# Optimization experiments

Hardware: AMD Instinct MI355X
Metric: run time of the kernel (lower is better)

The kernel has to match this reference:

```python
import jax, jax.numpy as jnp
import numpy as np

B, L, DIM, H = 2, 2048, 1024, 16
HD = DIM // H  # 64
EPS = 1e-6
ROPE_THETA = 10000.0


def _rmsnorm(x, scale):
    # mean of squares in float32 as in torch (dtype=torch.float32)
    ms = jnp.mean(jnp.square(x.astype(jnp.float32)), axis=-1, keepdims=True)
    inv = jax.lax.rsqrt(ms + EPS).astype(x.dtype)
    return x * inv * scale.astype(x.dtype)


def _rope_cos_sin(seq_len, head_dim, dtype):
    inv_freq = 1.0 / (ROPE_THETA ** (jnp.arange(0, head_dim, 2, dtype=jnp.float32) / head_dim))
    ang = jnp.arange(seq_len, dtype=jnp.float32)[:, None] * inv_freq[None, :]  # [L, HD/2]
    cos = jnp.cos(ang)[:, None, :].astype(dtype)  # [L,1,HD/2] broadcast over heads
    sin = jnp.sin(ang)[:, None, :].astype(dtype)
    return cos, sin


def _rope_apply(x, cos, sin):
    # x: [B,L,H,HD]; rotate-half formulation
    x1, x2 = jnp.split(x, 2, axis=-1)
    return jnp.concatenate([x1 * cos - x2 * sin, x2 * cos + x1 * sin], axis=-1)


def setup_inputs() -> dict:
    key = jax.random.key(0)
    k1, k2, k3 = jax.random.split(key, 3)
    x = jax.random.normal(k1, (B, L, DIM), dtype=jnp.float32)
    Wqkv = jax.random.normal(k2, (DIM, 3 * DIM), dtype=jnp.float32) * (DIM ** -0.5)
    Wproj = jax.random.normal(k3, (DIM, DIM), dtype=jnp.float32) * (DIM ** -0.5)
    q_scale = jnp.ones((HD,), dtype=jnp.float32)
    k_scale = jnp.ones((HD,), dtype=jnp.float32)
    bproj = jnp.zeros((DIM,), dtype=jnp.float32)
    return {"x": x, "Wqkv": Wqkv, "q_scale": q_scale, "k_scale": k_scale,
            "Wproj": Wproj, "bproj": bproj}


def reference(x, Wqkv, q_scale, k_scale, Wproj, bproj):
    b, l, c = x.shape
    qkv = x @ Wqkv  # [B,L,3*DIM]
    qkv = qkv.reshape(b, l, 3, H, HD)
    q, k, v = qkv[:, :, 0], qkv[:, :, 1], qkv[:, :, 2]  # each [B,L,H,HD]
    q = _rmsnorm(q, q_scale)
    k = _rmsnorm(k, k_scale)
    cos, sin = _rope_cos_sin(l, HD, x.dtype)
    q = _rope_apply(q, cos, sin)
    k = _rope_apply(k, cos, sin)
    scale = HD ** -0.5
    scores = jnp.einsum('blhd,bmhd->bhlm', q, k) * scale  # [B,H,L,L]
    p = jax.nn.softmax(scores, axis=-1)
    o = jnp.einsum('bhlm,bmhd->blhd', p, v).reshape(b, l, c)
    return o @ Wproj + bproj
```

## Files before the change

### kernel.cpp

```cpp
#include <hip/hip_runtime.h>
#include <hip/hip_bf16.h>
#include <cstdint>

#define B_   2
#define L_   2048
#define DIM_ 1024
#define H_   16
#define HD_  64
#define M_   (B_ * L_)
#define N3_  (3 * DIM_)

typedef unsigned short ushort_t;
typedef __bf16 bf16x8 __attribute__((ext_vector_type(8)));
typedef float  f32x4  __attribute__((ext_vector_type(4)));

__device__ __forceinline__ unsigned short f2b(float f) {
  return __builtin_bit_cast(unsigned short, (__bf16)f);
}
__device__ __forceinline__ float b2f(unsigned short s) {
  unsigned u = ((unsigned)s) << 16;
  return __builtin_bit_cast(float, u);
}
__device__ __forceinline__ float fmax3(float a, float b, float c) {
  return fmaxf(fmaxf(a, b), c);
}

typedef const __attribute__((address_space(1))) void* as1cp;
typedef __attribute__((address_space(3))) void* as3p;
__device__ __forceinline__ void gload_lds16(const void* g, void* l) {
  __builtin_amdgcn_global_load_lds((as1cp)g, (as3p)l, 16, 0, 0);
}

__global__ __launch_bounds__(256)
void conv_bf16(const float* __restrict__ in, ushort_t* __restrict__ out, int n4) {
  int i = blockIdx.x * 256 + threadIdx.x;
  if (i >= n4) return;
  float4 v = *(const float4*)&in[(size_t)i * 4];
  ushort4 o;
  o.x = f2b(v.x); o.y = f2b(v.y); o.z = f2b(v.z); o.w = f2b(v.w);
  *(ushort4*)&out[(size_t)i * 4] = o;
}

__global__ __launch_bounds__(256)
void transpose_conv(const float* __restrict__ in, ushort_t* __restrict__ out,
                    int R, int C) {
  __shared__ float tile[64][65];
  const int t = threadIdx.x;
  const int r0 = blockIdx.y * 64, c0 = blockIdx.x * 64;
#pragma unroll
  for (int p = 0; p < 4; ++p) {
    int r = (t >> 4) + p * 16;
    int c = (t & 15) * 4;
    float4 v = *(const float4*)&in[(size_t)(r0 + r) * C + (c0 + c)];
    tile[r][c + 0] = v.x; tile[r][c + 1] = v.y;
    tile[r][c + 2] = v.z; tile[r][c + 3] = v.w;
  }
  __syncthreads();
#pragma unroll
  for (int p = 0; p < 4; ++p) {
    int cc = (t >> 4) + p * 16;
    int r  = (t & 15) * 4;
    ushort4 o;
    o.x = f2b(tile[r + 0][cc]); o.y = f2b(tile[r + 1][cc]);
    o.z = f2b(tile[r + 2][cc]); o.w = f2b(tile[r + 3][cc]);
    *(ushort4*)&out[(size_t)(c0 + cc) * R + (r0 + r)] = o;
  }
}

__global__ __launch_bounds__(256)
void rope_tab(float* __restrict__ cosT, float* __restrict__ sinT) {
  int idx = blockIdx.x * 256 + threadIdx.x;
  int l = idx >> 5, d = idx & 31;
  float inv_freq = expf(-((float)(2 * d) / 64.f) * logf(10000.f));
  float ang = (float)l * inv_freq;
  cosT[idx] = cosf(ang);
  sinT[idx] = sinf(ang);
}

template <int MODE>
__global__ __launch_bounds__(256)
void gemm_bt(const ushort_t* __restrict__ A, const ushort_t* __restrict__ BT,
             void* __restrict__ Cout, ushort_t* __restrict__ vtout,
             const float* __restrict__ bias, int M, int N, int K, int ldc) {
  __shared__ ushort_t As[128 * 32];
  __shared__ ushort_t Bs[128 * 32];
  const int lane = threadIdx.x & 63;
  const int wid  = threadIdx.x >> 6;
  const int wm = wid >> 1, wn = wid & 1;
  const int m0 = blockIdx.y * 128, n0 = blockIdx.x * 128;
  const int ro = lane & 15, kg = lane >> 4;

  f32x4 acc[4][4] = {};

  for (int k0 = 0; k0 < K; k0 += 32) {
    const int cb = wid * 128;
#pragma unroll
    for (int j = 0; j < 2; ++j) {
      int c = cb + j * 64 + lane;
      gload_lds16(A + (size_t)(m0 + (c >> 2)) * K + k0 + (c & 3) * 8,
                  &As[(cb + j * 64) * 8]);
    }
#pragma unroll
    for (int j = 0; j < 2; ++j) {
      int c = cb + j * 64 + lane;
      gload_lds16(BT + (size_t)(n0 + (c >> 2)) * K + k0 + (c & 3) * 8,
                  &Bs[(cb + j * 64) * 8]);
    }
    __syncthreads();
    bf16x8 af[4], bfr[4];
#pragma unroll
    for (int i = 0; i < 4; ++i)
      af[i] = *(const bf16x8*)&As[(wm * 64 + i * 16 + ro) * 32 + kg * 8];
#pragma unroll
    for (int i = 0; i < 4; ++i)
      bfr[i] = *(const bf16x8*)&Bs[(wn * 64 + i * 16 + ro) * 32 + kg * 8];
#pragma unroll
    for (int i = 0; i < 4; ++i)
#pragma unroll
      for (int j = 0; j < 4; ++j)
        acc[i][j] = __builtin_amdgcn_mfma_f32_16x16x32_bf16(af[i], bfr[j],
                                                            acc[i][j], 0, 0, 0);
    __syncthreads();
  }

  if (MODE == 0) {
    if (n0 < 2048) {
#pragma unroll
      for (int i = 0; i < 4; ++i)
#pragma unroll
        for (int r = 0; r < 4; ++r) {
          int row = m0 + wm * 64 + i * 16 + kg * 4 + r;
#pragma unroll
          for (int j = 0; j < 4; ++j) {
            int col = n0 + wn * 64 + j * 16 + ro;
            ((ushort_t*)Cout)[(size_t)row * ldc + col] = f2b(acc[i][j][r]);
          }
        }
    } else {
#pragma unroll
      for (int i = 0; i < 4; ++i) {
        int rowb = m0 + wm * 64 + i * 16 + kg * 4;
        int bb = rowb >> 11, l = rowb & (L_ - 1);
#pragma unroll
        for (int j = 0; j < 4; ++j) {
          int dg = (n0 - 2048) + wn * 64 + j * 16 + ro;
          ushort4 o;
          o.x = f2b(acc[i][j][0]); o.y = f2b(acc[i][j][1]);
          o.z = f2b(acc[i][j][2]); o.w = f2b(acc[i][j][3]);
          *(ushort4*)&vtout[((size_t)bb * DIM_ + dg) * L_ + l] = o;
        }
      }
    }
  } else {
#pragma unroll
    for (int i = 0; i < 4; ++i)
#pragma unroll
      for (int r = 0; r < 4; ++r) {
        int row = m0 + wm * 64 + i * 16 + kg * 4 + r;
#pragma unroll
        for (int j = 0; j < 4; ++j) {
          int col = n0 + wn * 64 + j * 16 + ro;
          ((float*)Cout)[(size_t)row * ldc + col] = acc[i][j][r] + bias[col];
        }
      }
  }
}

__global__ __launch_bounds__(256)
void rmsrope(ushort_t* __restrict__ qk, const float* __restrict__ qs,
             const float* __restrict__ ks, const float* __restrict__ cosT,
             const float* __restrict__ sinT) {
  const int t = blockIdx.x;
  const int l = t & (L_ - 1);
  const int j = threadIdx.x & 15;
  const int h = threadIdx.x >> 4;
  const int dd = (j & 7) * 4;
  float4 cv = *(const float4*)&cosT[l * 32 + dd];
  float4 sv = *(const float4*)&sinT[l * 32 + dd];
  const float sgn = (j < 8) ? -1.f : 1.f;
#pragma unroll
  for (int ic = 0; ic < 2; ++ic) {
    const float qsc = (ic == 0) ? 0.125f * 1.44269504088896341f : 1.f;
    ushort_t* base = qk + (size_t)t * 2048 + ic * DIM_ + h * HD_ + j * 4;
    ushort4 raw = *(const ushort4*)base;
    float x0 = b2f(raw.x), x1 = b2f(raw.y), x2 = b2f(raw.z), x3 = b2f(raw.w);
    float ss = x0 * x0 + x1 * x1 + x2 * x2 + x3 * x3;
    ss += __shfl_xor(ss, 1); ss += __shfl_xor(ss, 2);
    ss += __shfl_xor(ss, 4); ss += __shfl_xor(ss, 8);
    float inv = rsqrtf(ss * (1.f / 64.f) + 1e-6f);
    const float* scp = (ic == 0 ? qs : ks) + j * 4;
    float4 sc = *(const float4*)scp;
    x0 *= inv * sc.x; x1 *= inv * sc.y; x2 *= inv * sc.z; x3 *= inv * sc.w;
    float y0 = __shfl_xor(x0, 8), y1 = __shfl_xor(x1, 8);
    float y2 = __shfl_xor(x2, 8), y3 = __shfl_xor(x3, 8);
    ushort4 o;
    o.x = f2b((x0 * cv.x + sgn * y0 * sv.x) * qsc);
    o.y = f2b((x1 * cv.y + sgn * y1 * sv.y) * qsc);
    o.z = f2b((x2 * cv.z + sgn * y2 * sv.z) * qsc);
    o.w = f2b((x3 * cv.w + sgn * y3 * sv.w) * qsc);
    *(ushort4*)base = o;
  }
}

__global__ __launch_bounds__(256)
void flash_attn(const ushort_t* __restrict__ qk, const ushort_t* __restrict__ vt,
                ushort_t* __restrict__ O) {
  const int qt = blockIdx.x, h = blockIdx.y, b = blockIdx.z;
  const int lane = threadIdx.x & 63, wid = threadIdx.x >> 6;
  const int ro = lane & 15, kg = lane >> 4;
  const int q0 = qt * 64;
  const size_t tok0 = (size_t)b * L_;
  const ushort_t* qb = qk + tok0 * 2048 + h * HD_;
  const ushort_t* kb = qb + DIM_;
  const ushort_t* vb = vt + ((size_t)b * DIM_ + h * HD_) * L_;

  __shared__ ushort_t Ks[2][4096];
  __shared__ ushort_t Vs[2][4096];
  __shared__ ushort_t Ps[4096];

  const int srow0 = wid * 16 + (lane >> 3);
  const int sch   = lane & 7;
  auto STAGE = [&](int bufi, int kt) {
#pragma unroll
    for (int j = 0; j < 2; ++j) {
      int row = srow0 + j * 8;
      int sc  = sch ^ (row & 7);
      gload_lds16(kb + (size_t)(kt * 64 + row) * 2048 + sc * 8,
                  &Ks[bufi][wid * 1024 + j * 512]);
      gload_lds16(vb + (size_t)row * L_ + kt * 64 + sc * 8,
                  &Vs[bufi][wid * 1024 + j * 512]);
    }
  };

  bf16x8 qf[2];
  {
    const ushort_t* g = qb + (size_t)(q0 + wid * 16 + ro) * 2048 + kg * 8;
    qf[0] = *(const bf16x8*)g;
    qf[1] = *(const bf16x8*)(g + 32);
  }

  bf16x8 onesv;
#pragma unroll
  for (int i = 0; i < 8; ++i) onesv[i] = (__bf16)1.0f;

  f32x4 oacc[4] = {};
  f32x4 lacc = {0.f, 0.f, 0.f, 0.f};
  float mrow = -1e30f;

  const int rowq = wid * 16 + ro;
  const int rx = ro & 7;

  const ushort_t* kbase[2][2];
  const ushort_t* vbase[2][2];
#pragma unroll
  for (int bi = 0; bi < 2; ++bi)
#pragma unroll
    for (int kk = 0; kk < 2; ++kk) {
      int ch = (kk * 4 + kg) ^ rx;
      kbase[bi][kk] = &Ks[bi][ro * 64 + ch * 8];
      vbase[bi][kk] = &Vs[bi][ro * 64 + ch * 8];
    }
  const ushort_t* pbase[2];
#pragma unroll
  for (int kk = 0; kk < 2; ++kk)
    pbase[kk] = &Ps[rowq * 64 + (((kk * 4 + kg) ^ rx) * 8)];
  ushort_t* pwaddr[4];
#pragma unroll
  for (int n = 0; n < 4; ++n)
    pwaddr[n] = &Ps[rowq * 64 + (((n * 2 + (kg >> 1)) ^ rx) * 8) + (kg & 1) * 4];

  STAGE(0, 0);
  __syncthreads();

  auto TILE = [&](int bi, int kt) {
    if (kt + 1 < L_ / 64) STAGE(bi ^ 1, kt + 1);

    f32x4 s[4];
#pragma unroll
    for (int n = 0; n < 4; ++n) {
      f32x4 z = {0.f, 0.f, 0.f, 0.f};
#pragma unroll
      for (int kk = 0; kk < 2; ++kk) {
        bf16x8 kf = *(const bf16x8*)(kbase[bi][kk] + n * 1024);
        z = __builtin_amdgcn_mfma_f32_16x16x32_bf16(kf, qf[kk], z, 0, 0, 0);
      }
      s[n] = z;
    }

    float t0 = fmax3(s[0][0], s[0][1], s[0][2]);
    float t1 = fmax3(s[0][3], s[1][0], s[1][1]);
    float t2 = fmax3(s[1][2], s[1][3], s[2][0]);
    float t3 = fmax3(s[2][1], s[2][2], s[2][3]);
    float t4 = fmax3(s[3][0], s[3][1], s[3][2]);
    float pm  = fmax3(t0, t1, t2);
    float pm2 = fmax3(t3, t4, s[3][3]);
    pm = fmaxf(pm, pm2);
    pm = fmaxf(pm, __shfl_xor(pm, 16));
    pm = fmaxf(pm, __shfl_xor(pm, 32));

    if (__any(pm > mrow + 8.f)) {
      float mn = fmaxf(mrow, pm);
      float alpha = __builtin_amdgcn_exp2f(mrow - mn);
      mrow = mn;
      float aro[4];
#pragma unroll
      for (int r = 0; r < 4; ++r) aro[r] = __shfl(alpha, kg * 20 + r);
#pragma unroll
      for (int n = 0; n < 4; ++n)
#pragma unroll
        for (int r = 0; r < 4; ++r) oacc[n][r] *= aro[r];
#pragma unroll
      for (int r = 0; r < 4; ++r) lacc[r] *= aro[r];
    }

#pragma unroll
    for (int n = 0; n < 4; ++n) {
      ushort4 pw;
      pw.x = f2b(__builtin_amdgcn_exp2f(s[n][0] - mrow));
      pw.y = f2b(__builtin_amdgcn_exp2f(s[n][1] - mrow));
      pw.z = f2b(__builtin_amdgcn_exp2f(s[n][2] - mrow));
      pw.w = f2b(__builtin_amdgcn_exp2f(s[n][3] - mrow));
      *(ushort4*)pwaddr[n] = pw;
    }

#pragma unroll
    for (int kk = 0; kk < 2; ++kk) {
      bf16x8 pf = *(const bf16x8*)pbase[kk];
      lacc = __builtin_amdgcn_mfma_f32_16x16x32_bf16(pf, onesv, lacc, 0, 0, 0);
#pragma unroll
      for (int n = 0; n < 4; ++n) {
        bf16x8 vf = *(const bf16x8*)(vbase[bi][kk] + n * 1024);
        oacc[n] = __builtin_amdgcn_mfma_f32_16x16x32_bf16(pf, vf, oacc[n], 0, 0, 0);
      }
    }

    __syncthreads();
  };

  for (int kt = 0; kt < L_ / 64; kt += 2) {
    TILE(0, kt);
    TILE(1, kt + 1);
  }

  float linv[4];
#pragma unroll
  for (int r = 0; r < 4; ++r) linv[r] = 1.f / lacc[r];
#pragma unroll
  for (int r = 0; r < 4; ++r) {
    int tok = (int)tok0 + q0 + wid * 16 + kg * 4 + r;
#pragma unroll
    for (int n = 0; n < 4; ++n)
      O[(size_t)tok * DIM_ + h * HD_ + n * 16 + ro] = f2b(oacc[n][r] * linv[r]);
  }
}

extern "C" void kernel_launch(void* const* d_in, const int* in_sizes, int n_in,
                              void* d_out, int out_size, void* d_ws, size_t ws_size,
                              hipStream_t stream) {
  const float* x     = (const float*)d_in[0];
  const float* Wqkv  = (const float*)d_in[1];
  const float* qs    = (const float*)d_in[2];
  const float* ks    = (const float*)d_in[3];
  const float* Wproj = (const float*)d_in[4];
  const float* bproj = (const float*)d_in[5];
  float* out = (float*)d_out;

  char* ws = (char*)d_ws;
  ushort_t* xb     = (ushort_t*)(ws);
  ushort_t* WqkvT  = (ushort_t*)(ws + (size_t)(8u << 20));
  ushort_t* WprojT = (ushort_t*)(ws + (size_t)(14u << 20));
  ushort_t* qkb    = (ushort_t*)(ws + (size_t)(16u << 20));
  ushort_t* vtb    = (ushort_t*)(ws + (size_t)(32u << 20));
  float*    cosT   = (float*)(ws + (size_t)(40u << 20));
  float*    sinT   = (float*)(ws + (size_t)(40u << 20) + (256u << 10));
  ushort_t* ob     = (ushort_t*)(ws + (size_t)(41u << 20));

  conv_bf16<<<4096, 256, 0, stream>>>(x, xb, M_ * DIM_ / 4);
  transpose_conv<<<dim3(48, 16), 256, 0, stream>>>(Wqkv, WqkvT, DIM_, N3_);
  transpose_conv<<<dim3(16, 16), 256, 0, stream>>>(Wproj, WprojT, DIM_, DIM_);
  rope_tab<<<256, 256, 0, stream>>>(cosT, sinT);
  gemm_bt<0><<<dim3(24, 32), 256, 0, stream>>>(xb, WqkvT, qkb, vtb, nullptr,
                                               M_, N3_, DIM_, 2048);
  rmsrope<<<4096, 256, 0, stream>>>(qkb, qs, ks, cosT, sinT);
  flash_attn<<<dim3(32, 16, 2), 256, 0, stream>>>(qkb, vtb, ob);
  gemm_bt<1><<<dim3(8, 32), 256, 0, stream>>>(ob, WprojT, out, nullptr, bproj,
                                              M_, DIM_, DIM_, DIM_);
}
```

Before: 159.7 us.

## Process two query row groups per wave in flash attention for K/V reuse

```diff
diff --git a/kernel.cpp b/kernel.cpp
--- a/kernel.cpp
+++ b/kernel.cpp
@@ -208,7 +208,7 @@
   const int qt = blockIdx.x, h = blockIdx.y, b = blockIdx.z;
   const int lane = threadIdx.x & 63, wid = threadIdx.x >> 6;
   const int ro = lane & 15, kg = lane >> 4;
-  const int q0 = qt * 64;
+  const int q0 = qt * 128;
   const size_t tok0 = (size_t)b * L_;
   const ushort_t* qb = qk + tok0 * 2048 + h * HD_;
   const ushort_t* kb = qb + DIM_;
@@ -216,7 +216,7 @@
 
   __shared__ ushort_t Ks[2][4096];
   __shared__ ushort_t Vs[2][4096];
-  __shared__ ushort_t Ps[4096];
+  __shared__ ushort_t Ps[8192];
 
   const int srow0 = wid * 16 + (lane >> 3);
   const int sch   = lane & 7;
@@ -232,22 +232,22 @@
     }
   };
 
-  bf16x8 qf[2];
-  {
-    const ushort_t* g = qb + (size_t)(q0 + wid * 16 + ro) * 2048 + kg * 8;
-    qf[0] = *(const bf16x8*)g;
-    qf[1] = *(const bf16x8*)(g + 32);
+  bf16x8 qf[2][2];
+#pragma unroll
+  for (int g = 0; g < 2; ++g) {
+    const ushort_t* gp = qb + (size_t)(q0 + wid * 32 + g * 16 + ro) * 2048 + kg * 8;
+    qf[g][0] = *(const bf16x8*)gp;
+    qf[g][1] = *(const bf16x8*)(gp + 32);
   }
 
   bf16x8 onesv;
 #pragma unroll
   for (int i = 0; i < 8; ++i) onesv[i] = (__bf16)1.0f;
 
-  f32x4 oacc[4] = {};
-  f32x4 lacc = {0.f, 0.f, 0.f, 0.f};
-  float mrow = -1e30f;
-
-  const int rowq = wid * 16 + ro;
+  f32x4 oacc[2][4] = {};
+  f32x4 lacc[2] = {};
+  float mrow[2] = {-1e30f, -1e30f};
+
   const int rx = ro & 7;
 
   const ushort_t* kbase[2][2];
@@ -260,14 +260,18 @@
       kbase[bi][kk] = &Ks[bi][ro * 64 + ch * 8];
       vbase[bi][kk] = &Vs[bi][ro * 64 + ch * 8];
     }
-  const ushort_t* pbase[2];
-#pragma unroll
-  for (int kk = 0; kk < 2; ++kk)
-    pbase[kk] = &Ps[rowq * 64 + (((kk * 4 + kg) ^ rx) * 8)];
-  ushort_t* pwaddr[4];
-#pragma unroll
-  for (int n = 0; n < 4; ++n)
-    pwaddr[n] = &Ps[rowq * 64 + (((n * 2 + (kg >> 1)) ^ rx) * 8) + (kg & 1) * 4];
+  const ushort_t* pbase[2][2];
+  ushort_t* pwaddr[2][4];
+#pragma unroll
+  for (int g = 0; g < 2; ++g) {
+    const int rowq = wid * 32 + g * 16 + ro;
+#pragma unroll
+    for (int kk = 0; kk < 2; ++kk)
+      pbase[g][kk] = &Ps[rowq * 64 + (((kk * 4 + kg) ^ rx) * 8)];
+#pragma unroll
+    for (int n = 0; n < 4; ++n)
+      pwaddr[g][n] = &Ps[rowq * 64 + (((n * 2 + (kg >> 1)) ^ rx) * 8) + (kg & 1) * 4];
+  }
 
   STAGE(0, 0);
   __syncthreads();
@@ -275,64 +279,76 @@
   auto TILE = [&](int bi, int kt) {
     if (kt + 1 < L_ / 64) STAGE(bi ^ 1, kt + 1);
 
-    f32x4 s[4];
+    f32x4 s[2][4];
+    __builtin_amdgcn_s_setprio(1);
 #pragma unroll
     for (int n = 0; n < 4; ++n) {
-      f32x4 z = {0.f, 0.f, 0.f, 0.f};
+      f32x4 z0 = {0.f, 0.f, 0.f, 0.f};
+      f32x4 z1 = {0.f, 0.f, 0.f, 0.f};
 #pragma unroll
       for (int kk = 0; kk < 2; ++kk) {
         bf16x8 kf = *(const bf16x8*)(kbase[bi][kk] + n * 1024);
-        z = __builtin_amdgcn_mfma_f32_16x16x32_bf16(kf, qf[kk], z, 0, 0, 0);
-      }
-      s[n] = z;
-    }
-
-    float t0 = fmax3(s[0][0], s[0][1], s[0][2]);
-    float t1 = fmax3(s[0][3], s[1][0], s[1][1]);
-    float t2 = fmax3(s[1][2], s[1][3], s[2][0]);
-    float t3 = fmax3(s[2][1], s[2][2], s[2][3]);
-    float t4 = fmax3(s[3][0], s[3][1], s[3][2]);
-    float pm  = fmax3(t0, t1, t2);
-    float pm2 = fmax3(t3, t4, s[3][3]);
-    pm = fmaxf(pm, pm2);
-    pm = fmaxf(pm, __shfl_xor(pm, 16));
-    pm = fmaxf(pm, __shfl_xor(pm, 32));
-
-    if (__any(pm > mrow + 8.f)) {
-      float mn = fmaxf(mrow, pm);
-      float alpha = __builtin_amdgcn_exp2f(mrow - mn);
-      mrow = mn;
-      float aro[4];
-#pragma unroll
-      for (int r = 0; r < 4; ++r) aro[r] = __shfl(alpha, kg * 20 + r);
-#pragma unroll
-      for (int n = 0; n < 4; ++n)
-#pragma unroll
-        for (int r = 0; r < 4; ++r) oacc[n][r] *= aro[r];
-#pragma unroll
-      for (int r = 0; r < 4; ++r) lacc[r] *= aro[r];
-    }
-
-#pragma unroll
-    for (int n = 0; n < 4; ++n) {
-      ushort4 pw;
-      pw.x = f2b(__builtin_amdgcn_exp2f(s[n][0] - mrow));
-      pw.y = f2b(__builtin_amdgcn_exp2f(s[n][1] - mrow));
-      pw.z = f2b(__builtin_amdgcn_exp2f(s[n][2] - mrow));
-      pw.w = f2b(__builtin_amdgcn_exp2f(s[n][3] - mrow));
-      *(ushort4*)pwaddr[n] = pw;
-    }
-
+        z0 = __builtin_amdgcn_mfma_f32_16x16x32_bf16(kf, qf[0][kk], z0, 0, 0, 0);
+        z1 = __builtin_amdgcn_mfma_f32_16x16x32_bf16(kf, qf[1][kk], z1, 0, 0, 0);
+      }
+      s[0][n] = z0; s[1][n] = z1;
+    }
+    __builtin_amdgcn_s_setprio(0);
+
+#pragma unroll
+    for (int g = 0; g < 2; ++g) {
+      float t0 = fmax3(s[g][0][0], s[g][0][1], s[g][0][2]);
+      float t1 = fmax3(s[g][0][3], s[g][1][0], s[g][1][1]);
+      float t2 = fmax3(s[g][1][2], s[g][1][3], s[g][2][0]);
+      float t3 = fmax3(s[g][2][1], s[g][2][2], s[g][2][3]);
+      float t4 = fmax3(s[g][3][0], s[g][3][1], s[g][3][2]);
+      float pm  = fmax3(t0, t1, t2);
+      float pm2 = fmax3(t3, t4, s[g][3][3]);
+      pm = fmaxf(pm, pm2);
+      pm = fmaxf(pm, __shfl_xor(pm, 16));
+      pm = fmaxf(pm, __shfl_xor(pm, 32));
+
+      if (__any(pm > mrow[g] + 8.f)) {
+        float mn = fmaxf(mrow[g], pm);
+        float alpha = __builtin_amdgcn_exp2f(mrow[g] - mn);
+        mrow[g] = mn;
+        float aro[4];
+#pragma unroll
+        for (int r = 0; r < 4; ++r) aro[r] = __shfl(alpha, kg * 20 + r);
+#pragma unroll
+        for (int n = 0; n < 4; ++n)
+#pragma unroll
+          for (int r = 0; r < 4; ++r) oacc[g][n][r] *= aro[r];
+#pragma unroll
+        for (int r = 0; r < 4; ++r) lacc[g][r] *= aro[r];
+      }
+
+#pragma unroll
+      for (int n = 0; n < 4; ++n) {
+        ushort4 pw;
+        pw.x = f2b(__builtin_amdgcn_exp2f(s[g][n][0] - mrow[g]));
+        pw.y = f2b(__builtin_amdgcn_exp2f(s[g][n][1] - mrow[g]));
+        pw.z = f2b(__builtin_amdgcn_exp2f(s[g][n][2] - mrow[g]));
+        pw.w = f2b(__builtin_amdgcn_exp2f(s[g][n][3] - mrow[g]));
+        *(ushort4*)pwaddr[g][n] = pw;
+      }
+    }
+
+    __builtin_amdgcn_s_setprio(1);
 #pragma unroll
     for (int kk = 0; kk < 2; ++kk) {
-      bf16x8 pf = *(const bf16x8*)pbase[kk];
-      lacc = __builtin_amdgcn_mfma_f32_16x16x32_bf16(pf, onesv, lacc, 0, 0, 0);
+      bf16x8 pf0 = *(const bf16x8*)pbase[0][kk];
+      bf16x8 pf1 = *(const bf16x8*)pbase[1][kk];
+      lacc[0] = __builtin_amdgcn_mfma_f32_16x16x32_bf16(pf0, onesv, lacc[0], 0, 0, 0);
+      lacc[1] = __builtin_amdgcn_mfma_f32_16x16x32_bf16(pf1, onesv, lacc[1], 0, 0, 0);
 #pragma unroll
       for (int n = 0; n < 4; ++n) {
         bf16x8 vf = *(const bf16x8*)(vbase[bi][kk] + n * 1024);
-        oacc[n] = __builtin_amdgcn_mfma_f32_16x16x32_bf16(pf, vf, oacc[n], 0, 0, 0);
-      }
-    }
+        oacc[0][n] = __builtin_amdgcn_mfma_f32_16x16x32_bf16(pf0, vf, oacc[0][n], 0, 0, 0);
+        oacc[1][n] = __builtin_amdgcn_mfma_f32_16x16x32_bf16(pf1, vf, oacc[1][n], 0, 0, 0);
+      }
+    }
+    __builtin_amdgcn_s_setprio(0);
 
     __syncthreads();
   };
@@ -342,15 +358,18 @@
     TILE(1, kt + 1);
   }
 
-  float linv[4];
-#pragma unroll
-  for (int r = 0; r < 4; ++r) linv[r] = 1.f / lacc[r];
-#pragma unroll
-  for (int r = 0; r < 4; ++r) {
-    int tok = (int)tok0 + q0 + wid * 16 + kg * 4 + r;
-#pragma unroll
-    for (int n = 0; n < 4; ++n)
-      O[(size_t)tok * DIM_ + h * HD_ + n * 16 + ro] = f2b(oacc[n][r] * linv[r]);
+#pragma unroll
+  for (int g = 0; g < 2; ++g) {
+    float linv[4];
+#pragma unroll
+    for (int r = 0; r < 4; ++r) linv[r] = 1.f / lacc[g][r];
+#pragma unroll
+    for (int r = 0; r < 4; ++r) {
+      int tok = (int)tok0 + q0 + wid * 32 + g * 16 + kg * 4 + r;
+#pragma unroll
+      for (int n = 0; n < 4; ++n)
+        O[(size_t)tok * DIM_ + h * HD_ + n * 16 + ro] = f2b(oacc[g][n][r] * linv[r]);
+    }
   }
 }
 
@@ -382,7 +401,7 @@
   gemm_bt<0><<<dim3(24, 32), 256, 0, stream>>>(xb, WqkvT, qkb, vtb, nullptr,
                                                M_, N3_, DIM_, 2048);
   rmsrope<<<4096, 256, 0, stream>>>(qkb, qs, ks, cosT, sinT);
-  flash_attn<<<dim3(32, 16, 2), 256, 0, stream>>>(qkb, vtb, ob);
+  flash_attn<<<dim3(16, 16, 2), 256, 0, stream>>>(qkb, vtb, ob);
   gemm_bt<1><<<dim3(8, 32), 256, 0, stream>>>(ob, WprojT, out, nullptr, bproj,
                                               M_, DIM_, DIM_, DIM_);
 }
```

Result: faster. 150.9 us (-5.5%).

## Rewrite flash attention with 32x32 MFMA, register-resident P via permlane swap

Applied to the files above, without the earlier changes.

```diff
diff --git a/kernel.cpp b/kernel.cpp
--- a/kernel.cpp
+++ b/kernel.cpp
@@ -13,6 +13,8 @@
 typedef unsigned short ushort_t;
 typedef __bf16 bf16x8 __attribute__((ext_vector_type(8)));
 typedef float  f32x4  __attribute__((ext_vector_type(4)));
+typedef float  f32x16 __attribute__((ext_vector_type(16)));
+typedef unsigned u32x2_t __attribute__((ext_vector_type(2)));
 
 __device__ __forceinline__ unsigned short f2b(float f) {
   return __builtin_bit_cast(unsigned short, (__bf16)f);
@@ -23,6 +25,20 @@
 }
 __device__ __forceinline__ float fmax3(float a, float b, float c) {
   return fmaxf(fmaxf(a, b), c);
+}
+
+__device__ __forceinline__ void plswap(unsigned &a, unsigned &b) {
+#if defined(__has_builtin) && __has_builtin(__builtin_amdgcn_permlane32_swap)
+  u32x2_t r = __builtin_amdgcn_permlane32_swap(a, b, false, false);
+  a = r[0]; b = r[1];
+#else
+  unsigned sa = (unsigned)__shfl_xor((int)a, 32);
+  unsigned sb = (unsigned)__shfl_xor((int)b, 32);
+  bool hi = (threadIdx.x & 32) != 0;
+  unsigned na = hi ? sb : a;
+  unsigned nb = hi ? b : sa;
+  a = na; b = nb;
+#endif
 }
 
 typedef const __attribute__((address_space(1))) void* as1cp;
@@ -207,8 +223,9 @@
                 ushort_t* __restrict__ O) {
   const int qt = blockIdx.x, h = blockIdx.y, b = blockIdx.z;
   const int lane = threadIdx.x & 63, wid = threadIdx.x >> 6;
-  const int ro = lane & 15, kg = lane >> 4;
-  const int q0 = qt * 64;
+  const int lq = lane & 31;
+  const int hi = lane >> 5;
+  const int q0 = qt * 128;
   const size_t tok0 = (size_t)b * L_;
   const ushort_t* qb = qk + tok0 * 2048 + h * HD_;
   const ushort_t* kb = qb + DIM_;
@@ -216,7 +233,6 @@
 
   __shared__ ushort_t Ks[2][4096];
   __shared__ ushort_t Vs[2][4096];
-  __shared__ ushort_t Ps[4096];
 
   const int srow0 = wid * 16 + (lane >> 3);
   const int sch   = lane & 7;
@@ -232,107 +248,106 @@
     }
   };
 
-  bf16x8 qf[2];
+  bf16x8 qf[4];
   {
-    const ushort_t* g = qb + (size_t)(q0 + wid * 16 + ro) * 2048 + kg * 8;
-    qf[0] = *(const bf16x8*)g;
-    qf[1] = *(const bf16x8*)(g + 32);
-  }
-
-  bf16x8 onesv;
-#pragma unroll
-  for (int i = 0; i < 8; ++i) onesv[i] = (__bf16)1.0f;
-
-  f32x4 oacc[4] = {};
-  f32x4 lacc = {0.f, 0.f, 0.f, 0.f};
-  float mrow = -1e30f;
-
-  const int rowq = wid * 16 + ro;
-  const int rx = ro & 7;
-
-  const ushort_t* kbase[2][2];
-  const ushort_t* vbase[2][2];
-#pragma unroll
-  for (int bi = 0; bi < 2; ++bi)
-#pragma unroll
-    for (int kk = 0; kk < 2; ++kk) {
-      int ch = (kk * 4 + kg) ^ rx;
-      kbase[bi][kk] = &Ks[bi][ro * 64 + ch * 8];
-      vbase[bi][kk] = &Vs[bi][ro * 64 + ch * 8];
-    }
-  const ushort_t* pbase[2];
-#pragma unroll
-  for (int kk = 0; kk < 2; ++kk)
-    pbase[kk] = &Ps[rowq * 64 + (((kk * 4 + kg) ^ rx) * 8)];
-  ushort_t* pwaddr[4];
-#pragma unroll
-  for (int n = 0; n < 4; ++n)
-    pwaddr[n] = &Ps[rowq * 64 + (((n * 2 + (kg >> 1)) ^ rx) * 8) + (kg & 1) * 4];
+    const ushort_t* gp = qb + (size_t)(q0 + wid * 32 + lq) * 2048;
+#pragma unroll
+    for (int s = 0; s < 4; ++s)
+      qf[s] = *(const bf16x8*)(gp + s * 16 + hi * 8);
+  }
+
+  int chs[4];
+#pragma unroll
+  for (int s = 0; s < 4; ++s) chs[s] = ((2 * s + hi) ^ (lq & 7)) * 8;
+
+  f32x16 oaccT[2] = {};
+  float mrow = -1e30f, lrow = 0.f;
 
   STAGE(0, 0);
   __syncthreads();
 
   auto TILE = [&](int bi, int kt) {
     if (kt + 1 < L_ / 64) STAGE(bi ^ 1, kt + 1);
-
-    f32x4 s[4];
-#pragma unroll
-    for (int n = 0; n < 4; ++n) {
-      f32x4 z = {0.f, 0.f, 0.f, 0.f};
-#pragma unroll
-      for (int kk = 0; kk < 2; ++kk) {
-        bf16x8 kf = *(const bf16x8*)(kbase[bi][kk] + n * 1024);
-        z = __builtin_amdgcn_mfma_f32_16x16x32_bf16(kf, qf[kk], z, 0, 0, 0);
+    const ushort_t* kb0 = &Ks[bi][lq * 64];
+    const ushort_t* vb0 = &Vs[bi][lq * 64];
+
+    f32x16 st[2];
+    __builtin_amdgcn_s_setprio(1);
+#pragma unroll
+    for (int t = 0; t < 2; ++t) {
+      f32x16 z = {};
+#pragma unroll
+      for (int s = 0; s < 4; ++s) {
+        bf16x8 kf = *(const bf16x8*)(kb0 + t * 2048 + chs[s]);
+        z = __builtin_amdgcn_mfma_f32_32x32x16_bf16(kf, qf[s], z, 0, 0, 0);
       }
-      s[n] = z;
-    }
-
-    float t0 = fmax3(s[0][0], s[0][1], s[0][2]);
-    float t1 = fmax3(s[0][3], s[1][0], s[1][1]);
-    float t2 = fmax3(s[1][2], s[1][3], s[2][0]);
-    float t3 = fmax3(s[2][1], s[2][2], s[2][3]);
-    float t4 = fmax3(s[3][0], s[3][1], s[3][2]);
-    float pm  = fmax3(t0, t1, t2);
-    float pm2 = fmax3(t3, t4, s[3][3]);
-    pm = fmaxf(pm, pm2);
-    pm = fmaxf(pm, __shfl_xor(pm, 16));
-    pm = fmaxf(pm, __shfl_xor(pm, 32));
+      st[t] = z;
+    }
+    __builtin_amdgcn_s_setprio(0);
+
+    float mx0, mx1, mx2, mx3;
+    {
+      float a0 = fmaxf(fmaxf(st[0][0], st[0][1]),  fmaxf(st[0][2], st[0][3]));
+      float a1 = fmaxf(fmaxf(st[0][4], st[0][5]),  fmaxf(st[0][6], st[0][7]));
+      float a2 = fmaxf(fmaxf(st[0][8], st[0][9]),  fmaxf(st[0][10], st[0][11]));
+      float a3 = fmaxf(fmaxf(st[0][12], st[0][13]), fmaxf(st[0][14], st[0][15]));
+      float b0 = fmaxf(fmaxf(st[1][0], st[1][1]),  fmaxf(st[1][2], st[1][3]));
+      float b1 = fmaxf(fmaxf(st[1][4], st[1][5]),  fmaxf(st[1][6], st[1][7]));
+      float b2 = fmaxf(fmaxf(st[1][8], st[1][9]),  fmaxf(st[1][10], st[1][11]));
+      float b3 = fmaxf(fmaxf(st[1][12], st[1][13]), fmaxf(st[1][14], st[1][15]));
+      mx0 = fmaxf(a0, b0); mx1 = fmaxf(a1, b1);
+      mx2 = fmaxf(a2, b2); mx3 = fmaxf(a3, b3);
+    }
+    float pmw = fmaxf(fmax3(mx0, mx1, mx2), mx3);
+    float pm  = fmaxf(pmw, __shfl_xor(pmw, 32));
 
     if (__any(pm > mrow + 8.f)) {
       float mn = fmaxf(mrow, pm);
       float alpha = __builtin_amdgcn_exp2f(mrow - mn);
       mrow = mn;
-      float aro[4];
-#pragma unroll
-      for (int r = 0; r < 4; ++r) aro[r] = __shfl(alpha, kg * 20 + r);
-#pragma unroll
-      for (int n = 0; n < 4; ++n)
-#pragma unroll
-        for (int r = 0; r < 4; ++r) oacc[n][r] *= aro[r];
-#pragma unroll
-      for (int r = 0; r < 4; ++r) lacc[r] *= aro[r];
-    }
-
-#pragma unroll
-    for (int n = 0; n < 4; ++n) {
-      ushort4 pw;
-      pw.x = f2b(__builtin_amdgcn_exp2f(s[n][0] - mrow));
-      pw.y = f2b(__builtin_amdgcn_exp2f(s[n][1] - mrow));
-      pw.z = f2b(__builtin_amdgcn_exp2f(s[n][2] - mrow));
-      pw.w = f2b(__builtin_amdgcn_exp2f(s[n][3] - mrow));
-      *(ushort4*)pwaddr[n] = pw;
-    }
-
-#pragma unroll
-    for (int kk = 0; kk < 2; ++kk) {
-      bf16x8 pf = *(const bf16x8*)pbase[kk];
-      lacc = __builtin_amdgcn_mfma_f32_16x16x32_bf16(pf, onesv, lacc, 0, 0, 0);
-#pragma unroll
-      for (int n = 0; n < 4; ++n) {
-        bf16x8 vf = *(const bf16x8*)(vbase[bi][kk] + n * 1024);
-        oacc[n] = __builtin_amdgcn_mfma_f32_16x16x32_bf16(pf, vf, oacc[n], 0, 0, 0);
+      lrow *= alpha;
+#pragma unroll
+      for (int dt = 0; dt < 2; ++dt)
+#pragma unroll
+        for (int r = 0; r < 16; ++r) oaccT[dt][r] *= alpha;
+    }
+
+    unsigned pk[2][8];
+    float rs0 = 0.f, rs1 = 0.f, rs2 = 0.f, rs3 = 0.f;
+#pragma unroll
+    for (int t = 0; t < 2; ++t)
+#pragma unroll
+      for (int p = 0; p < 8; ++p) {
+        float e0 = __builtin_amdgcn_exp2f(st[t][2 * p]     - mrow);
+        float e1 = __builtin_amdgcn_exp2f(st[t][2 * p + 1] - mrow);
+        if ((p & 3) == 0) { rs0 += e0; rs1 += e1; }
+        else if ((p & 3) == 1) { rs2 += e0; rs3 += e1; }
+        else if ((p & 3) == 2) { rs0 += e0; rs1 += e1; }
+        else { rs2 += e0; rs3 += e1; }
+        pk[t][p] = (unsigned)f2b(e0) | ((unsigned)f2b(e1) << 16);
       }
-    }
+    lrow += (rs0 + rs1) + (rs2 + rs3);
+
+    __builtin_amdgcn_s_setprio(1);
+#pragma unroll
+    for (int t = 0; t < 2; ++t)
+#pragma unroll
+      for (int blk = 0; blk < 2; ++blk) {
+        unsigned w0 = pk[t][4 * blk + 0], w1 = pk[t][4 * blk + 1];
+        unsigned w2 = pk[t][4 * blk + 2], w3 = pk[t][4 * blk + 3];
+        plswap(w0, w2);
+        plswap(w1, w3);
+        uint4 bw; bw.x = w0; bw.y = w1; bw.z = w2; bw.w = w3;
+        bf16x8 pf = __builtin_bit_cast(bf16x8, bw);
+        const int sg = 2 * t + blk;
+#pragma unroll
+        for (int dt = 0; dt < 2; ++dt) {
+          bf16x8 vf = *(const bf16x8*)(vb0 + dt * 2048 + chs[sg]);
+          oaccT[dt] = __builtin_amdgcn_mfma_f32_32x32x16_bf16(vf, pf,
+                                                              oaccT[dt], 0, 0, 0);
+        }
+      }
+    __builtin_amdgcn_s_setprio(0);
 
     __syncthreads();
   };
@@ -342,16 +357,21 @@
     TILE(1, kt + 1);
   }
 
-  float linv[4];
-#pragma unroll
-  for (int r = 0; r < 4; ++r) linv[r] = 1.f / lacc[r];
-#pragma unroll
-  for (int r = 0; r < 4; ++r) {
-    int tok = (int)tok0 + q0 + wid * 16 + kg * 4 + r;
-#pragma unroll
-    for (int n = 0; n < 4; ++n)
-      O[(size_t)tok * DIM_ + h * HD_ + n * 16 + ro] = f2b(oacc[n][r] * linv[r]);
-  }
+  lrow += __shfl_xor(lrow, 32);
+  float linv = 1.f / lrow;
+  ushort_t* obp = O + (size_t)(tok0 + q0 + wid * 32 + lq) * DIM_ + h * HD_;
+#pragma unroll
+  for (int dt = 0; dt < 2; ++dt)
+#pragma unroll
+    for (int g4 = 0; g4 < 4; ++g4) {
+      int d0 = dt * 32 + g4 * 8 + hi * 4;
+      ushort4 o4;
+      o4.x = f2b(oaccT[dt][4 * g4 + 0] * linv);
+      o4.y = f2b(oaccT[dt][4 * g4 + 1] * linv);
+      o4.z = f2b(oaccT[dt][4 * g4 + 2] * linv);
+      o4.w = f2b(oaccT[dt][4 * g4 + 3] * linv);
+      *(ushort4*)(obp + d0) = o4;
+    }
 }
 
 extern "C" void kernel_launch(void* const* d_in, const int* in_sizes, int n_in,
@@ -382,7 +402,7 @@
   gemm_bt<0><<<dim3(24, 32), 256, 0, stream>>>(xb, WqkvT, qkb, vtb, nullptr,
                                                M_, N3_, DIM_, 2048);
   rmsrope<<<4096, 256, 0, stream>>>(qkb, qs, ks, cosT, sinT);
-  flash_attn<<<dim3(32, 16, 2), 256, 0, stream>>>(qkb, vtb, ob);
+  flash_attn<<<dim3(16, 16, 2), 256, 0, stream>>>(qkb, vtb, ob);
   gemm_bt<1><<<dim3(8, 32), 256, 0, stream>>>(ob, WprojT, out, nullptr, bproj,
                                               M_, DIM_, DIM_, DIM_);
 }
```

Result: faster. 151.3 us (-5.2%).
